# Kernel tuning notes

Hardware: AMD Instinct MI355X
Metric: run time of the kernel (lower is better)

## Reference

```python
import jax, jax.numpy as jnp
import numpy as np

NUM_HEADS = 16
DIM = 2048
SEQ = 2048
ROPE_BASE = 10000.0
EPS = 1.1920929e-07  # torch.finfo(float32).eps, F.rms_norm default


def rms_norm(x):
    return x * jax.lax.rsqrt(jnp.mean(x * x, axis=-1, keepdims=True) + EPS)


def rotary(x):
    # x: [B, T, H, Dh]; rotate halves with per-position freqs
    B, T, H, Dh = x.shape
    inv_freq = (1.0 / ROPE_BASE) ** (jnp.arange(0, Dh, 2, dtype=jnp.float32) / Dh)
    freqs = jnp.arange(T, dtype=jnp.float32)[:, None] * inv_freq[None, :]  # [T, Dh/2]
    cos = jnp.cos(freqs)[None, :, None, :]
    sin = jnp.sin(freqs)[None, :, None, :]
    x1, x2 = jnp.split(x, 2, axis=-1)
    y1 = x1 * cos + x2 * sin
    y2 = -x1 * sin + x2 * cos
    return jnp.concatenate([y1, y2], axis=-1).astype(x.dtype)


def setup_inputs() -> dict:
    key = jax.random.key(0)
    ks = jax.random.split(key, 7)
    s = 1.0 / np.sqrt(DIM)
    return {
        "x": jax.random.normal(ks[0], (1, SEQ, DIM), dtype=jnp.float32),
        "vi": jax.random.normal(ks[1], (1, SEQ, DIM), dtype=jnp.float32),
        "wq": jax.random.normal(ks[2], (DIM, DIM), dtype=jnp.float32) * s,
        "wk": jax.random.normal(ks[3], (DIM, DIM), dtype=jnp.float32) * s,
        "wv": jax.random.normal(ks[4], (DIM, DIM), dtype=jnp.float32) * s,
        "wproj": jax.random.normal(ks[5], (DIM, DIM), dtype=jnp.float32) * s,
        "lambdas": jax.random.uniform(ks[6], (2,), dtype=jnp.float32),
    }


def reference(x, vi, wq, wk, wv, wproj, lambdas):
    B, T, D = x.shape
    H = NUM_HEADS
    Dh = D // H
    # CastedLinear: F.linear(x, W) == x @ W.T, no bias
    q = (x @ wq.T).reshape(B, T, H, Dh)
    k = (x @ wk.T).reshape(B, T, H, Dh)
    v = (x @ wv.T).reshape(B, T, H, Dh)
    v = lambdas[0] * v + lambdas[1] * vi.reshape(B, T, H, Dh)
    q, k = rms_norm(q), rms_norm(k)
    q, k = rotary(q), rotary(k)
    # causal attention (block_mask in source is causal), scale = 1/sqrt(Dh)
    scores = jnp.einsum("bthd,bshd->bhts", q, k) / jnp.sqrt(jnp.float32(Dh))
    causal = jnp.tril(jnp.ones((T, T), dtype=bool))
    scores = jnp.where(causal[None, None, :, :], scores, jnp.float32(-1e30))
    attn = jax.nn.softmax(scores, axis=-1)
    y = jnp.einsum("bhts,bshd->bthd", attn, v).reshape(B, T, D)
    return y @ wproj.T
```

## Files before the change

### kernel.cpp

```cpp
#include <hip/hip_runtime.h>

#define TSEQ 2048
#define DM   2048
#define NHEAD 16

typedef __bf16 bf16x8 __attribute__((ext_vector_type(8)));
typedef float  f32x4  __attribute__((ext_vector_type(4)));
typedef unsigned short ushort8v __attribute__((ext_vector_type(8)));
typedef unsigned int u32x4v __attribute__((ext_vector_type(4)));
typedef const __attribute__((address_space(1))) void* gas_cvp;
typedef __attribute__((address_space(3))) void* las_vp;

__device__ __forceinline__ unsigned short f2bf(float f) {
  unsigned int u = __builtin_bit_cast(unsigned int, f);
  u += 0x7FFFu + ((u >> 16) & 1u);
  return (unsigned short)(u >> 16);
}
__device__ __forceinline__ float bf2f(unsigned short u) {
  return __builtin_bit_cast(float, (unsigned int)u << 16);
}

__global__ __launch_bounds__(256) void cvt5(const float* __restrict__ x,
                                            const float* __restrict__ wq,
                                            const float* __restrict__ wk,
                                            const float* __restrict__ wv,
                                            const float* __restrict__ wp,
                                            unsigned short* __restrict__ xb,
                                            unsigned short* __restrict__ wqkvb,
                                            unsigned short* __restrict__ wpb) {
  const int NEL = DM * TSEQ;
  int gid = blockIdx.x * 256 + threadIdx.x;
  int seg = gid >> 19;
  int i = gid & ((1 << 19) - 1);
  const float* src;
  unsigned short* dst;
  switch (seg) {
    case 0: src = x;  dst = xb;                      break;
    case 1: src = wq; dst = wqkvb;                   break;
    case 2: src = wk; dst = wqkvb + (size_t)NEL;     break;
    case 3: src = wv; dst = wqkvb + (size_t)2 * NEL; break;
    default: src = wp; dst = wpb;                    break;
  }
  const float4* p = (const float4*)src + (size_t)i * 2;
  float4 a = p[0], b = p[1];
  ushort8v o;
  o[0] = f2bf(a.x); o[1] = f2bf(a.y); o[2] = f2bf(a.z); o[3] = f2bf(a.w);
  o[4] = f2bf(b.x); o[5] = f2bf(b.y); o[6] = f2bf(b.z); o[7] = f2bf(b.w);
  *((ushort8v*)dst + i) = o;
}

__global__ __launch_bounds__(512, 2) void gemm_qkv(const unsigned short* __restrict__ A,
                                                   const unsigned short* __restrict__ B,
                                                   unsigned short* __restrict__ C) {
  constexpr int TB = (256 + 192) * 128;
  __shared__ char lds[2 * TB];

  int orig = blockIdx.x;
  int swz = (orig & 7) * 32 + (orig >> 3);
  int bx = swz & 31, by = swz >> 5;
  int tileM = by * 256, tileN = bx * 192;

  int tid = threadIdx.x, w = tid >> 6, lane = tid & 63;
  int l15 = lane & 15, l4 = lane >> 4;
  int wm = w >> 1, wn = w & 1;
  int xorsw = (l15 & 7) << 4;
  int srow = tid >> 3, scolb = (tid & 7) * 16;

  const char* Ag = (const char*)A;
  const char* Bg = (const char*)B;

  f32x4 acc[4][6] = {};

  auto stageA = [&](int kt, int bsel) {
    char* dst0 = lds + bsel * TB + srow * 128 + scolb;
    #pragma unroll
    for (int i = 0; i < 4; ++i) {
      int row = i * 64 + srow;
      const char* src = Ag + (size_t)(tileM + row) * 4096
                        + kt * 128 + (scolb ^ ((row & 7) << 4));
      __builtin_amdgcn_global_load_lds((gas_cvp)src, (las_vp)(dst0 + i * 8192), 16, 0, 0);
    }
  };
  auto stageB = [&](int kt, int bsel) {
    char* dst0 = lds + bsel * TB + 32768 + srow * 128 + scolb;
    #pragma unroll
    for (int i = 0; i < 3; ++i) {
      int row = i * 64 + srow;
      const char* src = Bg + (size_t)(tileN + row) * 4096
                        + kt * 128 + (scolb ^ ((row & 7) << 4));
      __builtin_amdgcn_global_load_lds((gas_cvp)src, (las_vp)(dst0 + i * 8192), 16, 0, 0);
    }
  };

  stageA(0, 0);
  stageB(0, 0);
  #pragma unroll 2
  for (int t = 0; t < 32; ++t) {
    int buf = t & 1;
    const char* Lb = lds + buf * TB;
    bool pf = (t + 1 < 32);

    asm volatile("s_waitcnt vmcnt(3)" ::: "memory");
    __builtin_amdgcn_s_barrier();
    asm volatile("" ::: "memory");

    bf16x8 a[4][2], b[6][2];
    #pragma unroll
    for (int mf = 0; mf < 4; ++mf)
      #pragma unroll
      for (int kk = 0; kk < 2; ++kk)
        a[mf][kk] = *(const bf16x8*)(Lb + (wm * 64 + mf * 16 + l15) * 128 + ((kk * 64 + l4 * 16) ^ xorsw));
    if (pf) stageA(t + 1, buf ^ 1);

    if (pf) { asm volatile("s_waitcnt vmcnt(4)" ::: "memory"); }
    else    { asm volatile("s_waitcnt vmcnt(0)" ::: "memory"); }
    __builtin_amdgcn_s_barrier();
    asm volatile("" ::: "memory");

    #pragma unroll
    for (int nf = 0; nf < 6; ++nf)
      #pragma unroll
      for (int kk = 0; kk < 2; ++kk)
        b[nf][kk] = *(const bf16x8*)(Lb + 32768 + (wn * 96 + nf * 16 + l15) * 128 + ((kk * 64 + l4 * 16) ^ xorsw));
    if (pf) stageB(t + 1, buf ^ 1);

    __builtin_amdgcn_s_setprio(1);
    #pragma unroll
    for (int kk = 0; kk < 2; ++kk)
      #pragma unroll
      for (int mf = 0; mf < 4; ++mf)
        #pragma unroll
        for (int nf = 0; nf < 6; ++nf)
          acc[mf][nf] = __builtin_amdgcn_mfma_f32_16x16x32_bf16(a[mf][kk], b[nf][kk], acc[mf][nf], 0, 0, 0);
    __builtin_amdgcn_s_setprio(0);
  }

  #pragma unroll
  for (int mf = 0; mf < 4; ++mf) {
    int r0 = tileM + wm * 64 + mf * 16 + l4 * 4;
    #pragma unroll
    for (int nf = 0; nf < 6; ++nf) {
      int c0 = tileN + wn * 96 + nf * 16 + l15;
      #pragma unroll
      for (int j = 0; j < 4; ++j)
        C[(size_t)(r0 + j) * 6144 + c0] = f2bf(acc[mf][nf][j]);
    }
  }
}

__global__ __launch_bounds__(512, 2) void gemm_proj(const unsigned short* __restrict__ A,
                                                    const unsigned short* __restrict__ B,
                                                    float* __restrict__ C) {
  constexpr int TB = 256 * 128;
  __shared__ char lds[3 * TB];

  int orig = blockIdx.x;
  int swz = (orig & 7) * 32 + (orig >> 3);
  int bx = swz & 15, by = swz >> 4;
  int tileM = by * 128, tileN = bx * 128;

  int tid = threadIdx.x, w = tid >> 6, lane = tid & 63;
  int l15 = lane & 15, l4 = lane >> 4;
  int wm = w >> 2, wn = (w >> 1) & 1, ks = w & 1;
  int xorsw = (l15 & 7) << 4;
  int srow = tid >> 3, scolb = (tid & 7) * 16;
  int kb = ks * 64;

  const char* Ag = (const char*)A;
  const char* Bg = (const char*)B;

  f32x4 acc[4][4] = {};

  auto stage = [&](int kt, int bsel) {
    char* dst0 = lds + bsel * TB + srow * 128 + scolb;
    #pragma unroll
    for (int i = 0; i < 4; ++i) {
      int row = i * 64 + srow;
      const char* src = (row < 128 ? Ag + (size_t)(tileM + row) * 4096
                                   : Bg + (size_t)(tileN + row - 128) * 4096)
                        + kt * 128 + (scolb ^ ((row & 7) << 4));
      __builtin_amdgcn_global_load_lds((gas_cvp)src, (las_vp)(dst0 + i * 8192), 16, 0, 0);
    }
  };

  stage(0, 0);
  stage(1, 1);
  #pragma unroll 3
  for (int t = 0; t < 32; ++t) {
    int buf = t % 3;
    if (t + 1 < 32) { asm volatile("s_waitcnt vmcnt(4)" ::: "memory"); }
    else            { asm volatile("s_waitcnt vmcnt(0)" ::: "memory"); }
    __builtin_amdgcn_s_barrier();
    __builtin_amdgcn_sched_barrier(0);
    if (t + 2 < 32) stage(t + 2, (t + 2) % 3);

    const char* Lb = lds + buf * TB;
    bf16x8 a[4], b[4];
    #pragma unroll
    for (int mf = 0; mf < 4; ++mf)
      a[mf] = *(const bf16x8*)(Lb + (wm * 64 + mf * 16 + l15) * 128 + ((kb + l4 * 16) ^ xorsw));
    #pragma unroll
    for (int nf = 0; nf < 4; ++nf)
      b[nf] = *(const bf16x8*)(Lb + (128 + wn * 64 + nf * 16 + l15) * 128 + ((kb + l4 * 16) ^ xorsw));
    #pragma unroll
    for (int mf = 0; mf < 4; ++mf)
      #pragma unroll
      for (int nf = 0; nf < 4; ++nf)
        acc[mf][nf] = __builtin_amdgcn_mfma_f32_16x16x32_bf16(a[mf], b[nf], acc[mf][nf], 0, 0, 0);
  }

  __syncthreads();
  int pair = w >> 1;
  if (ks == 1) {
    #pragma unroll
    for (int mf = 0; mf < 4; ++mf)
      #pragma unroll
      for (int nf = 0; nf < 4; ++nf)
        *(f32x4*)(lds + pair * 16384 + ((mf * 4 + nf) * 64 + lane) * 16) = acc[mf][nf];
  }
  __syncthreads();
  if (ks == 0) {
    #pragma unroll
    for (int mf = 0; mf < 4; ++mf) {
      int r0 = tileM + wm * 64 + mf * 16 + l4 * 4;
      #pragma unroll
      for (int nf = 0; nf < 4; ++nf) {
        f32x4 o = acc[mf][nf] + *(const f32x4*)(lds + pair * 16384 + ((mf * 4 + nf) * 64 + lane) * 16);
        int c0 = tileN + wn * 64 + nf * 16 + l15;
        #pragma unroll
        for (int j = 0; j < 4; ++j)
          C[(size_t)(r0 + j) * 2048 + c0] = o[j];
      }
    }
  }
}

__global__ __launch_bounds__(256) void qkv_post(const unsigned short* __restrict__ qkv,
                                                const float* __restrict__ vi,
                                                const float* __restrict__ lam,
                                                unsigned short* __restrict__ qb,
                                                unsigned short* __restrict__ kb,
                                                unsigned short* __restrict__ vb) {
  int wid = blockIdx.x * 4 + (threadIdx.x >> 6);
  int lane = threadIdx.x & 63;
  int t = wid >> 4, h = wid & 15;
  const unsigned short* base = qkv + (size_t)t * (3 * DM) + h * 128;
  float l0 = lam[0], l1 = lam[1];

  float invf = exp2f((float)lane * -0.20762050593046014f);
  float ang = (float)t * invf;
  float sn, cs;
  sincosf(ang, &sn, &cs);

  size_t ob = (size_t)t * DM + h * 128;
  {
    float a = bf2f(base[lane]), b = bf2f(base[lane + 64]);
    float ss = a * a + b * b;
    #pragma unroll
    for (int m = 1; m < 64; m <<= 1) ss += __shfl_xor(ss, m, 64);
    float sc = rsqrtf(ss * (1.0f / 128.0f) + 1.1920929e-07f);
    a *= sc; b *= sc;
    qb[ob + lane]      = f2bf(a * cs + b * sn);
    qb[ob + 64 + lane] = f2bf(b * cs - a * sn);
  }
  {
    float a = bf2f(base[2048 + lane]), b = bf2f(base[2048 + 64 + lane]);
    float ss = a * a + b * b;
    #pragma unroll
    for (int m = 1; m < 64; m <<= 1) ss += __shfl_xor(ss, m, 64);
    float sc = rsqrtf(ss * (1.0f / 128.0f) + 1.1920929e-07f);
    a *= sc; b *= sc;
    kb[ob + lane]      = f2bf(a * cs + b * sn);
    kb[ob + 64 + lane] = f2bf(b * cs - a * sn);
  }
  {
    const float* vib = vi + (size_t)t * DM + h * 128;
    vb[ob + lane]      = f2bf(l0 * bf2f(base[4096 + lane])      + l1 * vib[lane]);
    vb[ob + 64 + lane] = f2bf(l0 * bf2f(base[4096 + 64 + lane]) + l1 * vib[lane + 64]);
  }
}

__global__ __launch_bounds__(256) void transpose_v(const unsigned short* __restrict__ vb,
                                                   unsigned short* __restrict__ vbT) {
  __shared__ __align__(16) unsigned short tile[64][68];
  int t0 = blockIdx.x * 64, d0 = blockIdx.y * 64, h = blockIdx.z;
  int tid = threadIdx.x;
  int li = tid >> 4;
  int lj = (tid & 15) * 4;
  #pragma unroll
  for (int p = 0; p < 4; ++p) {
    int i = p * 16 + li;
    ushort4 v = *(const ushort4*)(vb + (size_t)(t0 + i) * DM + h * 128 + d0 + lj);
    tile[i][lj] = v.x; tile[i][lj + 1] = v.y; tile[i][lj + 2] = v.z; tile[i][lj + 3] = v.w;
  }
  __syncthreads();
  #pragma unroll
  for (int p = 0; p < 4; ++p) {
    int j = p * 16 + li;
    ushort4 wv;
    wv.x = tile[lj][j]; wv.y = tile[lj + 1][j]; wv.z = tile[lj + 2][j]; wv.w = tile[lj + 3][j];
    *(ushort4*)(vbT + (size_t)h * 128 * TSEQ + (size_t)(d0 + j) * TSEQ + t0 + lj) = wv;
  }
}

__global__ __launch_bounds__(512, 2) void attn_split(const unsigned short* __restrict__ qb,
                                                     const unsigned short* __restrict__ kb,
                                                     const unsigned short* __restrict__ vbT,
                                                     unsigned short* __restrict__ O01,
                                                     unsigned short* __restrict__ O23,
                                                     float2* __restrict__ ml) {
  __shared__ __align__(16) char Ks[2][16384];
  __shared__ __align__(16) char Vs[2][16384];

  int bi = blockIdx.x;
  int qblk = 7 - (bi >> 6);
  int h = (bi >> 2) & 15;
  int s = bi & 3;
  int len = qblk + 1;
  int st0 = s * len, st1 = st0 + len;

  int tid = threadIdx.x, w = tid >> 6, lane = tid & 63;
  int l15 = lane & 15, l4 = lane >> 4;
  int qr0 = qblk * 256 + w * 32;
  int xorK = (l15 & 7) << 4;
  int srcA = ((((l4 << 1)) & 3) * 16 + l15) << 2;
  int srcB = ((((l4 << 1) + 1) & 3) * 16 + l15) << 2;
  bool hi4 = (l4 >> 1) != 0;

  bf16x8 q_frag[2][4];
  #pragma unroll
  for (int qt = 0; qt < 2; ++qt) {
    const unsigned short* qrow = qb + (size_t)(qr0 + qt * 16 + l15) * DM + h * 128 + l4 * 8;
    #pragma unroll
    for (int kk = 0; kk < 4; ++kk) q_frag[qt][kk] = *(const bf16x8*)(qrow + kk * 32);
  }

  const char* kbase = (const char*)kb + (size_t)h * 256;
  const char* vbase = (const char*)vbT + (size_t)h * 128 * TSEQ * 2;

  f32x4 acc_o[2][8] = {};
  float mrow[2] = {-1e30f, -1e30f};
  float lrow[2] = {0.f, 0.f};
  const float scale = 0.08838834764831845f;

  auto stage = [&](int st, int bsel) {
    const char* kb1 = kbase + (size_t)st * 64 * 4096;
    const char* vb1 = vbase + (size_t)st * 64 * 2;
    #pragma unroll
    for (int it = 0; it < 2; ++it) {
      int L = (it * 512 + tid) * 16;
      int row = L >> 8, b = L & 255;
      const char* src = kb1 + (size_t)row * 4096 + (b ^ ((row & 7) << 4));
      __builtin_amdgcn_global_load_lds((gas_cvp)src, (las_vp)(&Ks[bsel][0] + L), 16, 0, 0);
    }
    #pragma unroll
    for (int it = 0; it < 2; ++it) {
      int L = (it * 512 + tid) * 16;
      int row = L >> 7, b = L & 127;
      const char* src = vb1 + (size_t)row * (TSEQ * 2) + (b ^ ((row & 7) << 4));
      __builtin_amdgcn_global_load_lds((gas_cvp)src, (las_vp)(&Vs[bsel][0] + L), 16, 0, 0);
    }
  };

  stage(st0, 0);
  int buf = 0;

  for (int st = st0; st < st1; ++st) {
    asm volatile("s_waitcnt vmcnt(0) lgkmcnt(0)" ::: "memory");
    __builtin_amdgcn_s_barrier();
    __builtin_amdgcn_sched_barrier(0);
    if (st + 1 < st1) stage(st + 1, buf ^ 1);

    f32x4 acc_s[2][4] = {};
    __builtin_amdgcn_s_setprio(1);
    #pragma unroll
    for (int j = 0; j < 4; ++j) {
      const char* kr = &Ks[buf][0] + (j * 16 + l15) * 256;
      #pragma unroll
      for (int kk = 0; kk < 4; ++kk) {
        bf16x8 kf = *(const bf16x8*)(kr + ((l4 * 16 + kk * 64) ^ xorK));
        acc_s[0][j] = __builtin_amdgcn_mfma_f32_16x16x32_bf16(kf, q_frag[0][kk], acc_s[0][j], 0, 0, 0);
        acc_s[1][j] = __builtin_amdgcn_mfma_f32_16x16x32_bf16(kf, q_frag[1][kk], acc_s[1][j], 0, 0, 0);
      }
    }
    __builtin_amdgcn_s_setprio(0);

    int kv0 = st * 64;
    bool needmask = (kv0 + 63) > qr0;
    u32x4v pf[2][2];

    #pragma unroll
    for (int qt = 0; qt < 2; ++qt) {
      int qg = qr0 + qt * 16 + l15;
      float sv[4][4];
      float pmax = -1e30f;
      if (needmask) {
        #pragma unroll
        for (int j = 0; j < 4; ++j)
          #pragma unroll
          for (int r = 0; r < 4; ++r) {
            float v = acc_s[qt][j][r] * scale;
            if ((kv0 + j * 16 + l4 * 4 + r) > qg) v = -1e30f;
            sv[j][r] = v;
            pmax = fmaxf(pmax, v);
          }
      } else {
        #pragma unroll
        for (int j = 0; j < 4; ++j)
          #pragma unroll
          for (int r = 0; r < 4; ++r) {
            float v = acc_s[qt][j][r] * scale;
            sv[j][r] = v;
            pmax = fmaxf(pmax, v);
          }
      }
      pmax = fmaxf(pmax, __shfl_xor(pmax, 16, 64));
      pmax = fmaxf(pmax, __shfl_xor(pmax, 32, 64));

      if (!__all(pmax - mrow[qt] <= 8.0f)) {
        float mn = fmaxf(mrow[qt], pmax);
        float f = __expf(mrow[qt] - mn);
        mrow[qt] = mn;
        lrow[qt] *= f;
        #pragma unroll
        for (int n = 0; n < 8; ++n) acc_o[qt][n] *= f;
      }
      float mn = mrow[qt];

      float psum = 0.f;
      unsigned pk[4][2];
      #pragma unroll
      for (int j = 0; j < 4; ++j)
        #pragma unroll
        for (int rr = 0; rr < 2; ++rr) {
          float p0 = __expf(sv[j][2 * rr] - mn);
          float p1 = __expf(sv[j][2 * rr + 1] - mn);
          psum += p0 + p1;
          unsigned pkw;
          asm("v_cvt_pk_bf16_f32 %0, %1, %2" : "=v"(pkw) : "v"(p0), "v"(p1));
          pk[j][rr] = pkw;
        }
      psum += __shfl_xor(psum, 16, 64);
      psum += __shfl_xor(psum, 32, 64);
      lrow[qt] += psum;

      #pragma unroll
      for (int kk = 0; kk < 2; ++kk) {
        u32x4v pw;
        #pragma unroll
        for (int w2 = 0; w2 < 4; ++w2) {
          int rr = w2 & 1;
          int src = (w2 < 2) ? srcA : srcB;
          unsigned c0 = (unsigned)__builtin_amdgcn_ds_bpermute(src, (int)pk[2 * kk][rr]);
          unsigned c1 = (unsigned)__builtin_amdgcn_ds_bpermute(src, (int)pk[2 * kk + 1][rr]);
          pw[w2] = hi4 ? c1 : c0;
        }
        pf[qt][kk] = pw;
      }
    }

    __builtin_amdgcn_s_setprio(1);
    #pragma unroll
    for (int kk = 0; kk < 2; ++kk) {
      bf16x8 pb0 = __builtin_bit_cast(bf16x8, pf[0][kk]);
      bf16x8 pb1 = __builtin_bit_cast(bf16x8, pf[1][kk]);
      #pragma unroll
      for (int n = 0; n < 8; ++n) {
        bf16x8 vf = *(const bf16x8*)(&Vs[buf][0] + (n * 16 + l15) * 128 + ((kk * 64 + l4 * 16) ^ xorK));
        acc_o[0][n] = __builtin_amdgcn_mfma_f32_16x16x32_bf16(vf, pb0, acc_o[0][n], 0, 0, 0);
        acc_o[1][n] = __builtin_amdgcn_mfma_f32_16x16x32_bf16(vf, pb1, acc_o[1][n], 0, 0, 0);
      }
    }
    __builtin_amdgcn_s_setprio(0);
    buf ^= 1;
  }

  unsigned short* Op = (s < 2 ? O01 + (size_t)s * (TSEQ * DM)
                              : O23 + (size_t)(s - 2) * (TSEQ * DM));
  #pragma unroll
  for (int qt = 0; qt < 2; ++qt) {
    int q = qr0 + qt * 16 + l15;
    #pragma unroll
    for (int n = 0; n < 8; ++n) {
      ushort4 st4;
      st4.x = f2bf(acc_o[qt][n][0]);
      st4.y = f2bf(acc_o[qt][n][1]);
      st4.z = f2bf(acc_o[qt][n][2]);
      st4.w = f2bf(acc_o[qt][n][3]);
      *(ushort4*)(Op + (size_t)q * DM + h * 128 + n * 16 + l4 * 4) = st4;
    }
    if (l4 == 0)
      ml[(size_t)s * (TSEQ * NHEAD) + (size_t)q * NHEAD + h] = make_float2(mrow[qt], lrow[qt]);
  }
}

__global__ __launch_bounds__(256) void attn_combine(const unsigned short* __restrict__ O01,
                                                    const unsigned short* __restrict__ O23,
                                                    const float2* __restrict__ ml,
                                                    unsigned short* __restrict__ yb) {
  const int TN = TSEQ * NHEAD;
  int idx = blockIdx.x * 256 + threadIdx.x;
  int rowid = idx >> 5;
  float2 m0 = ml[rowid];
  float2 m1 = ml[TN + rowid];
  float2 m2 = ml[2 * TN + rowid];
  float2 m3 = ml[3 * TN + rowid];
  float m = fmaxf(fmaxf(m0.x, m1.x), fmaxf(m2.x, m3.x));
  float a0 = __expf(m0.x - m), a1 = __expf(m1.x - m);
  float a2 = __expf(m2.x - m), a3 = __expf(m3.x - m);
  float inv = 1.0f / (a0 * m0.y + a1 * m1.y + a2 * m2.y + a3 * m3.y);
  ushort4 o0 = ((const ushort4*)O01)[idx];
  ushort4 o1 = ((const ushort4*)(O01 + (size_t)TSEQ * DM))[idx];
  ushort4 o2 = ((const ushort4*)O23)[idx];
  ushort4 o3 = ((const ushort4*)(O23 + (size_t)TSEQ * DM))[idx];
  ushort4 r;
  r.x = f2bf((a0 * bf2f(o0.x) + a1 * bf2f(o1.x) + a2 * bf2f(o2.x) + a3 * bf2f(o3.x)) * inv);
  r.y = f2bf((a0 * bf2f(o0.y) + a1 * bf2f(o1.y) + a2 * bf2f(o2.y) + a3 * bf2f(o3.y)) * inv);
  r.z = f2bf((a0 * bf2f(o0.z) + a1 * bf2f(o1.z) + a2 * bf2f(o2.z) + a3 * bf2f(o3.z)) * inv);
  r.w = f2bf((a0 * bf2f(o0.w) + a1 * bf2f(o1.w) + a2 * bf2f(o2.w) + a3 * bf2f(o3.w)) * inv);
  *(ushort4*)(yb + (size_t)idx * 4) = r;
}

extern "C" void kernel_launch(void* const* d_in, const int* in_sizes, int n_in,
                              void* d_out, int out_size, void* d_ws, size_t ws_size,
                              hipStream_t stream) {
  const float* x   = (const float*)d_in[0];
  const float* vi  = (const float*)d_in[1];
  const float* wq  = (const float*)d_in[2];
  const float* wk  = (const float*)d_in[3];
  const float* wv  = (const float*)d_in[4];
  const float* wp  = (const float*)d_in[5];
  const float* lam = (const float*)d_in[6];

  const size_t MB = 1024 * 1024;
  const int NEL = DM * TSEQ;
  const int N8  = NEL / 8;
  char* ws = (char*)d_ws;
  unsigned short* xb    = (unsigned short*)(ws);
  unsigned short* wqkvb = (unsigned short*)(ws + 8  * MB);
  unsigned short* wpb   = (unsigned short*)(ws + 32 * MB);
  unsigned short* qkvb  = (unsigned short*)(ws + 40 * MB);
  unsigned short* O01   = (unsigned short*)(ws);
  unsigned short* O23   = (unsigned short*)(ws + 64 * MB);
  float2*         mlbuf = (float2*)(ws + 84 * MB);
  unsigned short* qb2   = (unsigned short*)(ws + 88 * MB);
  unsigned short* kb2   = (unsigned short*)(ws + 96 * MB);
  unsigned short* vb    = (unsigned short*)(ws + 104 * MB);
  unsigned short* vbT   = (unsigned short*)(ws + 112 * MB);
  unsigned short* yb    = (unsigned short*)(ws + 120 * MB);

  cvt5<<<5 * N8 / 256, 256, 0, stream>>>(x, wq, wk, wv, wp, xb, wqkvb, wpb);

  gemm_qkv<<<256, 512, 0, stream>>>(xb, wqkvb, qkvb);

  qkv_post<<<(TSEQ * NHEAD) / 4, 256, 0, stream>>>(qkvb, vi, lam, qb2, kb2, vb);

  transpose_v<<<dim3(TSEQ / 64, 2, NHEAD), 256, 0, stream>>>(vb, vbT);

  attn_split<<<512, 512, 0, stream>>>(qb2, kb2, vbT, O01, O23, mlbuf);
  attn_combine<<<(TSEQ * DM / 4) / 256, 256, 0, stream>>>(O01, O23, mlbuf, yb);

  gemm_proj<<<256, 512, 0, stream>>>(yb, wpb, (float*)d_out);
}
```

Before: 162.1 us.

## Restructure QKV GEMM main loop into quadrant-wise LDS reads interleaved with MFMA

Rewrites the QKV projection GEMM inner loop so each K-step splits the 4x6 MFMA tile into four 2x3 quadrants. LDS fragment reads for the next quadrant are interleaved between MFMA groups, and all seven global-to-LDS prefetch loads for the next K-tile are issued together. The goal is to overlap LDS reads with matrix-core work and lower peak fragment register pressure. The cost is several extra workgroup barriers per K-step and a full vmcnt(0) wait at the end of each iteration, which removes the previous partial-wait overlap of global loads.

```diff
diff --git a/kernel.cpp b/kernel.cpp
--- a/kernel.cpp
+++ b/kernel.cpp
@@ -70,69 +70,87 @@
   const char* Bg = (const char*)B;
 
   f32x4 acc[4][6] = {};
-
-  auto stageA = [&](int kt, int bsel) {
-    char* dst0 = lds + bsel * TB + srow * 128 + scolb;
+  bf16x8 a0[2][2], a1[2][2], b0[3][2], b1[3][2];
+
+  auto stage7 = [&](int kt, int bsel) {
+    char* dstA = lds + bsel * TB + srow * 128 + scolb;
     #pragma unroll
     for (int i = 0; i < 4; ++i) {
       int row = i * 64 + srow;
-      const char* src = Ag + (size_t)(tileM + row) * 4096
-                        + kt * 128 + (scolb ^ ((row & 7) << 4));
-      __builtin_amdgcn_global_load_lds((gas_cvp)src, (las_vp)(dst0 + i * 8192), 16, 0, 0);
-    }
-  };
-  auto stageB = [&](int kt, int bsel) {
-    char* dst0 = lds + bsel * TB + 32768 + srow * 128 + scolb;
+      const char* src = Ag + (size_t)(tileM + row) * 4096 + kt * 128 + (scolb ^ ((row & 7) << 4));
+      __builtin_amdgcn_global_load_lds((gas_cvp)src, (las_vp)(dstA + i * 8192), 16, 0, 0);
+    }
+    char* dstB = lds + bsel * TB + 32768 + srow * 128 + scolb;
     #pragma unroll
     for (int i = 0; i < 3; ++i) {
       int row = i * 64 + srow;
-      const char* src = Bg + (size_t)(tileN + row) * 4096
-                        + kt * 128 + (scolb ^ ((row & 7) << 4));
-      __builtin_amdgcn_global_load_lds((gas_cvp)src, (las_vp)(dst0 + i * 8192), 16, 0, 0);
+      const char* src = Bg + (size_t)(tileN + row) * 4096 + kt * 128 + (scolb ^ ((row & 7) << 4));
+      __builtin_amdgcn_global_load_lds((gas_cvp)src, (las_vp)(dstB + i * 8192), 16, 0, 0);
     }
   };
-
-  stageA(0, 0);
-  stageB(0, 0);
-  #pragma unroll 2
+  auto readAh = [&](bf16x8 (&ar)[2][2], int ah, const char* Lb) {
+    #pragma unroll
+    for (int mfl = 0; mfl < 2; ++mfl)
+      #pragma unroll
+      for (int kk = 0; kk < 2; ++kk) {
+        int row = wm * 64 + (ah * 2 + mfl) * 16 + l15;
+        ar[mfl][kk] = *(const bf16x8*)(Lb + row * 128 + ((kk * 64 + l4 * 16) ^ xorsw));
+      }
+  };
+  auto readBh = [&](bf16x8 (&br)[3][2], int bh, const char* Lb) {
+    #pragma unroll
+    for (int nfl = 0; nfl < 3; ++nfl)
+      #pragma unroll
+      for (int kk = 0; kk < 2; ++kk) {
+        int row = wn * 96 + (bh * 3 + nfl) * 16 + l15;
+        br[nfl][kk] = *(const bf16x8*)(Lb + 32768 + row * 128 + ((kk * 64 + l4 * 16) ^ xorsw));
+      }
+  };
+  auto mfma12 = [&](int ah, int bh, bf16x8 (&ar)[2][2], bf16x8 (&br)[3][2]) {
+    __builtin_amdgcn_s_setprio(1);
+    #pragma unroll
+    for (int kk = 0; kk < 2; ++kk)
+      #pragma unroll
+      for (int mfl = 0; mfl < 2; ++mfl)
+        #pragma unroll
+        for (int nfl = 0; nfl < 3; ++nfl)
+          acc[ah * 2 + mfl][bh * 3 + nfl] =
+            __builtin_amdgcn_mfma_f32_16x16x32_bf16(ar[mfl][kk], br[nfl][kk],
+                                                    acc[ah * 2 + mfl][bh * 3 + nfl], 0, 0, 0);
+    __builtin_amdgcn_s_setprio(0);
+  };
+
+  stage7(0, 0);
+  asm volatile("s_waitcnt vmcnt(0)" ::: "memory");
+  __builtin_amdgcn_s_barrier();
+  asm volatile("" ::: "memory");
+
   for (int t = 0; t < 32; ++t) {
-    int buf = t & 1;
-    const char* Lb = lds + buf * TB;
-    bool pf = (t + 1 < 32);
-
-    asm volatile("s_waitcnt vmcnt(3)" ::: "memory");
+    const char* Lb = lds + (t & 1) * TB;
+    readAh(a0, 0, Lb);
+    readBh(b0, 0, Lb);
+    if (t + 1 < 32) stage7(t + 1, (t & 1) ^ 1);
+    __builtin_amdgcn_s_barrier();
+    asm volatile("s_waitcnt lgkmcnt(0)" ::: "memory");
+    __builtin_amdgcn_sched_barrier(0);
+    mfma12(0, 0, a0, b0);
+    __builtin_amdgcn_s_barrier();
+    readBh(b1, 1, Lb);
+    __builtin_amdgcn_s_barrier();
+    asm volatile("s_waitcnt lgkmcnt(0)" ::: "memory");
+    __builtin_amdgcn_sched_barrier(0);
+    mfma12(0, 1, a0, b1);
+    __builtin_amdgcn_s_barrier();
+    readAh(a1, 1, Lb);
+    __builtin_amdgcn_s_barrier();
+    asm volatile("s_waitcnt lgkmcnt(0)" ::: "memory");
+    __builtin_amdgcn_sched_barrier(0);
+    mfma12(1, 1, a1, b1);
+    __builtin_amdgcn_s_barrier();
+    mfma12(1, 0, a1, b0);
+    asm volatile("s_waitcnt vmcnt(0)" ::: "memory");
     __builtin_amdgcn_s_barrier();
     asm volatile("" ::: "memory");
-
-    bf16x8 a[4][2], b[6][2];
-    #pragma unroll
-    for (int mf = 0; mf < 4; ++mf)
-      #pragma unroll
-      for (int kk = 0; kk < 2; ++kk)
-        a[mf][kk] = *(const bf16x8*)(Lb + (wm * 64 + mf * 16 + l15) * 128 + ((kk * 64 + l4 * 16) ^ xorsw));
-    if (pf) stageA(t + 1, buf ^ 1);
-
-    if (pf) { asm volatile("s_waitcnt vmcnt(4)" ::: "memory"); }
-    else    { asm volatile("s_waitcnt vmcnt(0)" ::: "memory"); }
-    __builtin_amdgcn_s_barrier();
-    asm volatile("" ::: "memory");
-
-    #pragma unroll
-    for (int nf = 0; nf < 6; ++nf)
-      #pragma unroll
-      for (int kk = 0; kk < 2; ++kk)
-        b[nf][kk] = *(const bf16x8*)(Lb + 32768 + (wn * 96 + nf * 16 + l15) * 128 + ((kk * 64 + l4 * 16) ^ xorsw));
-    if (pf) stageB(t + 1, buf ^ 1);
-
-    __builtin_amdgcn_s_setprio(1);
-    #pragma unroll
-    for (int kk = 0; kk < 2; ++kk)
-      #pragma unroll
-      for (int mf = 0; mf < 4; ++mf)
-        #pragma unroll
-        for (int nf = 0; nf < 6; ++nf)
-          acc[mf][nf] = __builtin_amdgcn_mfma_f32_16x16x32_bf16(a[mf][kk], b[nf][kk], acc[mf][nf], 0, 0, 0);
-    __builtin_amdgcn_s_setprio(0);
   }
 
   #pragma unroll
```

After: 169.6 us. +4.6%, slower.
